# Optimization experiments

Measured on AMD Instinct MI355X. Metric: run time of the kernel, lower is better.

## Reference

```python
import jax, jax.numpy as jnp
import numpy as np

N = 4096      # num nodes
FIN = 256     # num_in_features
H = 8         # num_of_heads
F = 64        # num_out_features per head
NEG = -1e9    # additive mask value for non-edges


def setup_inputs() -> dict:
    key = jax.random.key(0)
    ks = jax.random.split(key, 7)
    x = jax.random.normal(ks[0], (N, FIN), dtype=jnp.float32)
    adj = jax.random.bernoulli(ks[1], 0.01, (N, N)) | jnp.eye(N, dtype=bool)
    connectivity_mask = jnp.where(adj, 0.0, NEG).astype(jnp.float32)
    # Xavier-uniform-ish scaled params
    W = jax.random.normal(ks[2], (H * F, FIN), dtype=jnp.float32) * np.float32(1.0 / np.sqrt(FIN))
    a_src = jax.random.normal(ks[3], (1, H, F), dtype=jnp.float32) * np.float32(0.1)
    a_tgt = jax.random.normal(ks[4], (1, H, F), dtype=jnp.float32) * np.float32(0.1)
    skip_W = jax.random.normal(ks[5], (H * F, FIN), dtype=jnp.float32) * np.float32(1.0 / np.sqrt(FIN))
    bias = jnp.zeros((H * F,), dtype=jnp.float32)
    return {"x": x, "connectivity_mask": connectivity_mask, "W": W,
            "a_src": a_src, "a_tgt": a_tgt, "skip_W": skip_W, "bias": bias}


def reference(x, connectivity_mask, W, a_src, a_tgt, skip_W, bias):
    # linear_proj (no bias), view to [N, H, F]   (dropout omitted: eval mode)
    proj = (x @ W.T).reshape(N, H, F)
    # per-head scalar scores: [N, H] -> [H, N, 1] and [H, 1, N]
    s_src = jnp.sum(proj * a_src, axis=-1).T[:, :, None]   # [H, N, 1]
    s_tgt = jnp.sum(proj * a_tgt, axis=-1).T[:, None, :]   # [H, 1, N]
    scores = jax.nn.leaky_relu(s_src + s_tgt, negative_slope=0.2)  # [H, N, N]
    alpha = jax.nn.softmax(scores + connectivity_mask[None, :, :], axis=-1)
    # weighted aggregation: bmm(alpha, proj^T) then permute back to [N, H, F]
    out = jnp.einsum('hij,jhf->ihf', alpha, proj)
    # skip connection (dims differ: F_in=256 vs H*F output per head) -> skip_proj
    out = out + (x @ skip_W.T).reshape(N, H, F)
    # concat heads, add bias, ELU activation
    out = out.reshape(N, H * F) + bias
    return jax.nn.elu(out)
```

## Files before the change

### kernel.cpp

```cpp
#include <hip/hip_runtime.h>
#include <hip/hip_bf16.h>

#define NN 4096
#define FIN 256
#define NH 8
#define NF 64
#define HF 512
#define MAXD 128

typedef __attribute__((ext_vector_type(4))) float f32x4;
typedef unsigned short u16;
typedef unsigned int u32;

__device__ __forceinline__ u16 f2bf(float x) {
    u32 u = __float_as_uint(x);
    u += 0x7fffu + ((u >> 16) & 1u);
    return (u16)(u >> 16);
}

__global__ __launch_bounds__(256) void gemm64(
    const float* __restrict__ X,
    const float* __restrict__ B0, const float* __restrict__ B1,
    float* __restrict__ C0, float* __restrict__ C1,
    u16* __restrict__ projh)
{
    const float* Bp = blockIdx.z ? B1 : B0;
    float* Cp = blockIdx.z ? C1 : C0;
    const int bm = blockIdx.y * 64, bn = blockIdx.x * 64;
    __shared__ float As[32][68];
    __shared__ float Bs[32][68];
    const int t = threadIdx.x;
    const int tx = t & 15, ty = t >> 4;
    const int r = t >> 2, kq = (t & 3) * 8;
    f32x4 acc[4] = {};
    for (int k0 = 0; k0 < FIN; k0 += 32) {
        const float4 av0 = *(const float4*)&X[(bm + r) * FIN + k0 + kq];
        const float4 av1 = *(const float4*)&X[(bm + r) * FIN + k0 + kq + 4];
        const float4 bv0 = *(const float4*)&Bp[(bn + r) * FIN + k0 + kq];
        const float4 bv1 = *(const float4*)&Bp[(bn + r) * FIN + k0 + kq + 4];
        __syncthreads();
        As[kq+0][r]=av0.x; As[kq+1][r]=av0.y; As[kq+2][r]=av0.z; As[kq+3][r]=av0.w;
        As[kq+4][r]=av1.x; As[kq+5][r]=av1.y; As[kq+6][r]=av1.z; As[kq+7][r]=av1.w;
        Bs[kq+0][r]=bv0.x; Bs[kq+1][r]=bv0.y; Bs[kq+2][r]=bv0.z; Bs[kq+3][r]=bv0.w;
        Bs[kq+4][r]=bv1.x; Bs[kq+5][r]=bv1.y; Bs[kq+6][r]=bv1.z; Bs[kq+7][r]=bv1.w;
        __syncthreads();
        #pragma unroll
        for (int k = 0; k < 32; ++k) {
            const f32x4 a4 = *(const f32x4*)&As[k][ty * 4];
            const f32x4 b4 = *(const f32x4*)&Bs[k][tx * 4];
            acc[0] += a4.x * b4;
            acc[1] += a4.y * b4;
            acc[2] += a4.z * b4;
            acc[3] += a4.w * b4;
        }
    }
    #pragma unroll
    for (int i = 0; i < 4; ++i)
        *(f32x4*)&Cp[(size_t)(bm + ty * 4 + i) * HF + bn + tx * 4] = acc[i];
    if (blockIdx.z == 0) {
        #pragma unroll
        for (int i = 0; i < 4; ++i) {
            union { u16 h[4]; uint2 v; } pk;
            #pragma unroll
            for (int q = 0; q < 4; ++q) pk.h[q] = f2bf(acc[i][q]);
            *(uint2*)&projh[(size_t)(bm + ty * 4 + i) * HF + bn + tx * 4] = pk.v;
        }
    }
}

__global__ __launch_bounds__(256) void s_kernel(
    const float* __restrict__ proj, const float* __restrict__ a_src,
    const float* __restrict__ a_tgt, float* __restrict__ s_src,
    float* __restrict__ s_tgt)
{
    const int wg = (blockIdx.x * 256 + threadIdx.x) >> 6;
    const int lane = threadIdx.x & 63;
    const int i = wg >> 3, h = wg & 7;
    const float v = proj[(size_t)i * HF + h * NF + lane];
    float ps = v * a_src[h * NF + lane];
    float pt = v * a_tgt[h * NF + lane];
    #pragma unroll
    for (int off = 32; off; off >>= 1) {
        ps += __shfl_xor(ps, off);
        pt += __shfl_xor(pt, off);
    }
    if (lane == 0) { s_src[h * NN + i] = ps; s_tgt[h * NN + i] = pt; }
}

__global__ __launch_bounds__(256) void sparse_attn(
    const float* __restrict__ mask, const u16* __restrict__ projh,
    const float* __restrict__ s_src, const float* __restrict__ s_tgt,
    const float* __restrict__ skipv, const float* __restrict__ bias,
    float* __restrict__ out)
{
    const int i = blockIdx.x;
    const int t = threadIdx.x;
    __shared__ int nbr[MAXD];
    __shared__ float alpha_s[NH][MAXD];
    __shared__ int cnt_s;
    if (t == 0) cnt_s = 0;
    __syncthreads();

    const float4* mrow = (const float4*)&mask[(size_t)i * NN];
    #pragma unroll
    for (int it = 0; it < 4; ++it) {
        const float4 v = mrow[it * 256 + t];
        const int j0 = (it * 256 + t) * 4;
        if (v.x > -0.5f) { int p = atomicAdd(&cnt_s, 1); if (p < MAXD) nbr[p] = j0; }
        if (v.y > -0.5f) { int p = atomicAdd(&cnt_s, 1); if (p < MAXD) nbr[p] = j0 + 1; }
        if (v.z > -0.5f) { int p = atomicAdd(&cnt_s, 1); if (p < MAXD) nbr[p] = j0 + 2; }
        if (v.w > -0.5f) { int p = atomicAdd(&cnt_s, 1); if (p < MAXD) nbr[p] = j0 + 3; }
    }
    __syncthreads();
    const int cnt = min(cnt_s, MAXD);

    {
        const int h = t >> 5, l = t & 31;
        const float ss = s_src[h * NN + i];
        float sc[4]; float m = -1e30f;
        #pragma unroll
        for (int q = 0; q < 4; ++q) {
            const int k = l + 32 * q;
            if (k < cnt) {
                float s = ss + s_tgt[h * NN + nbr[k]];
                s = s > 0.f ? s : 0.2f * s;
                sc[q] = s; m = fmaxf(m, s);
            } else sc[q] = -1e30f;
        }
        #pragma unroll
        for (int off = 16; off; off >>= 1) m = fmaxf(m, __shfl_xor(m, off));
        float p[4]; float psum = 0.f;
        #pragma unroll
        for (int q = 0; q < 4; ++q) {
            p[q] = exp2f((sc[q] - m) * 1.4426950408889634f);
            psum += p[q];
        }
        #pragma unroll
        for (int off = 16; off; off >>= 1) psum += __shfl_xor(psum, off);
        const float inv = 1.0f / psum;
        #pragma unroll
        for (int q = 0; q < 4; ++q) {
            const int k = l + 32 * q;
            if (k < cnt) alpha_s[h][k] = p[q] * inv;
        }
    }
    __syncthreads();

    const int w = t >> 6, lane = t & 63;
    const int c = w * 128 + lane * 2;
    const int head = c >> 6;
    const u32* ph = (const u32*)projh;
    const int cidx = c >> 1;
    float acc0 = 0.f, acc1 = 0.f;
    int k = 0;
    for (; k + 2 <= cnt; k += 2) {
        const int j0 = nbr[k], j1 = nbr[k + 1];
        const float a0 = alpha_s[head][k], a1 = alpha_s[head][k + 1];
        const u32 v0 = ph[(size_t)j0 * 256 + cidx];
        const u32 v1 = ph[(size_t)j1 * 256 + cidx];
        acc0 += a0 * __uint_as_float(v0 << 16);
        acc1 += a0 * __uint_as_float(v0 & 0xffff0000u);
        acc0 += a1 * __uint_as_float(v1 << 16);
        acc1 += a1 * __uint_as_float(v1 & 0xffff0000u);
    }
    if (k < cnt) {
        const int j0 = nbr[k];
        const float a0 = alpha_s[head][k];
        const u32 v0 = ph[(size_t)j0 * 256 + cidx];
        acc0 += a0 * __uint_as_float(v0 << 16);
        acc1 += a0 * __uint_as_float(v0 & 0xffff0000u);
    }

    const float2 sk = *(const float2*)&skipv[(size_t)i * HF + c];
    const float2 bs = *(const float2*)&bias[c];
    float o0 = acc0 + sk.x + bs.x;
    float o1 = acc1 + sk.y + bs.y;
    o0 = o0 > 0.f ? o0 : expm1f(o0);
    o1 = o1 > 0.f ? o1 : expm1f(o1);
    *(float2*)&out[(size_t)i * HF + c] = make_float2(o0, o1);
}

extern "C" void kernel_launch(void* const* d_in, const int* in_sizes, int n_in,
                              void* d_out, int out_size, void* d_ws, size_t ws_size,
                              hipStream_t stream)
{
    (void)in_sizes; (void)n_in; (void)out_size; (void)ws_size;
    const float* x     = (const float*)d_in[0];
    const float* mask  = (const float*)d_in[1];
    const float* W     = (const float*)d_in[2];
    const float* a_src = (const float*)d_in[3];
    const float* a_tgt = (const float*)d_in[4];
    const float* skW   = (const float*)d_in[5];
    const float* bias  = (const float*)d_in[6];
    float* out = (float*)d_out;

    char* ws = (char*)d_ws;
    float* proj  = (float*)(ws);
    float* skipv = (float*)(ws + (8u << 20));
    u16*   projh = (u16*)(ws + (16u << 20));
    float* s_src = (float*)(ws + (20u << 20));
    float* s_tgt = (float*)(ws + (20u << 20) + 262144);

    gemm64<<<dim3(8, 64, 2), 256, 0, stream>>>(x, W, skW, proj, skipv, projh);
    s_kernel<<<dim3(8192), 256, 0, stream>>>(proj, a_src, a_tgt, s_src, s_tgt);
    sparse_attn<<<dim3(4096), 256, 0, stream>>>(mask, projh, s_src, s_tgt,
                                                skipv, bias, out);
}
```

Measured before the change: 169.3 us.

## Use bf16 MFMA GEMM, split mask scan from aggregation, unroll gather loop

Converts x and both weight matrices to bf16 and replaces the fp32 SIMT GEMM with a double-buffered MFMA 16x16x32 bf16 GEMM that loads tiles with global_load_lds. The fp32 proj buffer is dropped and the score kernel reads the bf16 projection instead. The mask scan moves into its own kernel that writes neighbour lists, and the aggregation loop is unrolled by 8 with padded entries so more gathers are in flight. This adds a conversion pass and bf16 rounding of the GEMM inputs, which lowers precision of proj, skip and the scores.

```diff
diff --git a/kernel.cpp b/kernel.cpp
--- a/kernel.cpp
+++ b/kernel.cpp
@@ -9,74 +9,140 @@
 #define MAXD 128
 
 typedef __attribute__((ext_vector_type(4))) float f32x4;
+typedef __attribute__((ext_vector_type(8))) short short8;
 typedef unsigned short u16;
 typedef unsigned int u32;
+
+union Frag { uint4 u; short8 s; };
 
 __device__ __forceinline__ u16 f2bf(float x) {
     u32 u = __float_as_uint(x);
     u += 0x7fffu + ((u >> 16) & 1u);
     return (u16)(u >> 16);
 }
-
-__global__ __launch_bounds__(256) void gemm64(
-    const float* __restrict__ X,
-    const float* __restrict__ B0, const float* __restrict__ B1,
-    float* __restrict__ C0, float* __restrict__ C1,
-    u16* __restrict__ projh)
-{
-    const float* Bp = blockIdx.z ? B1 : B0;
-    float* Cp = blockIdx.z ? C1 : C0;
-    const int bm = blockIdx.y * 64, bn = blockIdx.x * 64;
-    __shared__ float As[32][68];
-    __shared__ float Bs[32][68];
+__device__ __forceinline__ float bf2f(u32 lo16) {
+    return __uint_as_float(lo16 << 16);
+}
+
+__global__ __launch_bounds__(256) void cvt_kernel(
+    const float* __restrict__ x, const float* __restrict__ W,
+    const float* __restrict__ skW,
+    u16* __restrict__ xh, u16* __restrict__ Wh, u16* __restrict__ skWh)
+{
+    const int gid = blockIdx.x * 256 + threadIdx.x;
+    const float* src; u16* dst; int off;
+    if (gid < 131072)      { src = x;   dst = xh;   off = gid; }
+    else if (gid < 147456) { src = W;   dst = Wh;   off = gid - 131072; }
+    else                   { src = skW; dst = skWh; off = gid - 147456; }
+    const int e = off * 8;
+    const float4 a = *(const float4*)&src[e];
+    const float4 b = *(const float4*)&src[e + 4];
+    union { u16 h[8]; uint4 v; } pk;
+    pk.h[0]=f2bf(a.x); pk.h[1]=f2bf(a.y); pk.h[2]=f2bf(a.z); pk.h[3]=f2bf(a.w);
+    pk.h[4]=f2bf(b.x); pk.h[5]=f2bf(b.y); pk.h[6]=f2bf(b.z); pk.h[7]=f2bf(b.w);
+    *(uint4*)&dst[e] = pk.v;
+}
+
+__global__ __launch_bounds__(256) void gemm_mfma(
+    const u16* __restrict__ xh, const u16* __restrict__ Wh,
+    const u16* __restrict__ skWh,
+    u16* __restrict__ projh, float* __restrict__ skipv)
+{
+    const int z = blockIdx.z;
+    const u16* Bg = z ? skWh : Wh;
+    const int bm = blockIdx.y * 128, bn = blockIdx.x * 128;
+    __shared__ u16 lds[2][2][8192];
     const int t = threadIdx.x;
-    const int tx = t & 15, ty = t >> 4;
-    const int r = t >> 2, kq = (t & 3) * 8;
-    f32x4 acc[4] = {};
-    for (int k0 = 0; k0 < FIN; k0 += 32) {
-        const float4 av0 = *(const float4*)&X[(bm + r) * FIN + k0 + kq];
-        const float4 av1 = *(const float4*)&X[(bm + r) * FIN + k0 + kq + 4];
-        const float4 bv0 = *(const float4*)&Bp[(bn + r) * FIN + k0 + kq];
-        const float4 bv1 = *(const float4*)&Bp[(bn + r) * FIN + k0 + kq + 4];
+    const int w = t >> 6, lane = t & 63;
+    const int wm = w >> 1, wn = w & 1;
+    const int l15 = lane & 15, lk = lane >> 4;
+
+    f32x4 acc[4][4] = {};
+
+    auto stage = [&](int buf, int ks) {
+        const int k0 = ks * 64;
+        #pragma unroll
+        for (int q = 0; q < 4; ++q) {
+            const int s = q * 256 + t;
+            const int kk = s >> 9, fr = (s >> 6) & 7;
+            const int row = bm + fr * 16 + l15;
+            const int kel = k0 + kk * 32 + lk * 8;
+            u16* ldst = &lds[buf][0][(q * 256 + w * 64) * 8];
+            __builtin_amdgcn_global_load_lds(
+                (const __attribute__((address_space(1))) u32*)&xh[row * FIN + kel],
+                (__attribute__((address_space(3))) u32*)ldst, 16, 0, 0);
+        }
+        #pragma unroll
+        for (int q = 0; q < 4; ++q) {
+            const int s = q * 256 + t;
+            const int kk = s >> 9, fr = (s >> 6) & 7;
+            const int row = bn + fr * 16 + l15;
+            const int kel = k0 + kk * 32 + lk * 8;
+            u16* ldst = &lds[buf][1][(q * 256 + w * 64) * 8];
+            __builtin_amdgcn_global_load_lds(
+                (const __attribute__((address_space(1))) u32*)&Bg[row * FIN + kel],
+                (__attribute__((address_space(3))) u32*)ldst, 16, 0, 0);
+        }
+    };
+    auto compute = [&](int buf) {
+        const uint4* Ab = (const uint4*)&lds[buf][0][0];
+        const uint4* Bb = (const uint4*)&lds[buf][1][0];
+        #pragma unroll
+        for (int kk = 0; kk < 2; ++kk) {
+            Frag a[4], b[4];
+            #pragma unroll
+            for (int m = 0; m < 4; ++m) a[m].u = Ab[(kk * 8 + wm * 4 + m) * 64 + lane];
+            #pragma unroll
+            for (int n = 0; n < 4; ++n) b[n].u = Bb[(kk * 8 + wn * 4 + n) * 64 + lane];
+            #pragma unroll
+            for (int m = 0; m < 4; ++m)
+                #pragma unroll
+                for (int n = 0; n < 4; ++n)
+                    acc[m][n] = __builtin_amdgcn_mfma_f32_16x16x32_bf16(
+                        a[m].s, b[n].s, acc[m][n], 0, 0, 0);
+        }
+    };
+
+    stage(0, 0);
+    asm volatile("s_waitcnt vmcnt(0)" ::: "memory");
+    __syncthreads();
+    int buf = 0;
+    for (int ks = 0; ks < 4; ++ks) {
+        if (ks < 3) stage(buf ^ 1, ks + 1);
+        compute(buf);
+        asm volatile("s_waitcnt vmcnt(0)" ::: "memory");
         __syncthreads();
-        As[kq+0][r]=av0.x; As[kq+1][r]=av0.y; As[kq+2][r]=av0.z; As[kq+3][r]=av0.w;
-        As[kq+4][r]=av1.x; As[kq+5][r]=av1.y; As[kq+6][r]=av1.z; As[kq+7][r]=av1.w;
-        Bs[kq+0][r]=bv0.x; Bs[kq+1][r]=bv0.y; Bs[kq+2][r]=bv0.z; Bs[kq+3][r]=bv0.w;
-        Bs[kq+4][r]=bv1.x; Bs[kq+5][r]=bv1.y; Bs[kq+6][r]=bv1.z; Bs[kq+7][r]=bv1.w;
-        __syncthreads();
-        #pragma unroll
-        for (int k = 0; k < 32; ++k) {
-            const f32x4 a4 = *(const f32x4*)&As[k][ty * 4];
-            const f32x4 b4 = *(const f32x4*)&Bs[k][tx * 4];
-            acc[0] += a4.x * b4;
-            acc[1] += a4.y * b4;
-            acc[2] += a4.z * b4;
-            acc[3] += a4.w * b4;
-        }
-    }
+        buf ^= 1;
+    }
+
     #pragma unroll
-    for (int i = 0; i < 4; ++i)
-        *(f32x4*)&Cp[(size_t)(bm + ty * 4 + i) * HF + bn + tx * 4] = acc[i];
-    if (blockIdx.z == 0) {
-        #pragma unroll
-        for (int i = 0; i < 4; ++i) {
-            union { u16 h[4]; uint2 v; } pk;
-            #pragma unroll
-            for (int q = 0; q < 4; ++q) pk.h[q] = f2bf(acc[i][q]);
-            *(uint2*)&projh[(size_t)(bm + ty * 4 + i) * HF + bn + tx * 4] = pk.v;
+    for (int m = 0; m < 4; ++m) {
+        const int r0 = bm + wm * 64 + m * 16 + lk * 4;
+        #pragma unroll
+        for (int n = 0; n < 4; ++n) {
+            const int c = bn + wn * 64 + n * 16 + l15;
+            if (z == 0) {
+                #pragma unroll
+                for (int rr = 0; rr < 4; ++rr)
+                    projh[(size_t)(r0 + rr) * HF + c] = f2bf(acc[m][n][rr]);
+            } else {
+                #pragma unroll
+                for (int rr = 0; rr < 4; ++rr)
+                    skipv[(size_t)(r0 + rr) * HF + c] = acc[m][n][rr];
+            }
         }
     }
 }
 
 __global__ __launch_bounds__(256) void s_kernel(
-    const float* __restrict__ proj, const float* __restrict__ a_src,
+    const u16* __restrict__ projh, const float* __restrict__ a_src,
     const float* __restrict__ a_tgt, float* __restrict__ s_src,
     float* __restrict__ s_tgt)
 {
     const int wg = (blockIdx.x * 256 + threadIdx.x) >> 6;
     const int lane = threadIdx.x & 63;
     const int i = wg >> 3, h = wg & 7;
-    const float v = proj[(size_t)i * HF + h * NF + lane];
+    const float v = bf2f(projh[(size_t)i * HF + h * NF + lane]);
     float ps = v * a_src[h * NF + lane];
     float pt = v * a_tgt[h * NF + lane];
     #pragma unroll
@@ -87,32 +153,48 @@
     if (lane == 0) { s_src[h * NN + i] = ps; s_tgt[h * NN + i] = pt; }
 }
 
-__global__ __launch_bounds__(256) void sparse_attn(
-    const float* __restrict__ mask, const u16* __restrict__ projh,
-    const float* __restrict__ s_src, const float* __restrict__ s_tgt,
-    const float* __restrict__ skipv, const float* __restrict__ bias,
-    float* __restrict__ out)
-{
-    const int i = blockIdx.x;
-    const int t = threadIdx.x;
-    __shared__ int nbr[MAXD];
-    __shared__ float alpha_s[NH][MAXD];
+__global__ __launch_bounds__(256) void scan_kernel(
+    const float* __restrict__ mask, int* __restrict__ cnt_g,
+    int* __restrict__ nbr_g)
+{
+    const int i = blockIdx.x, t = threadIdx.x;
+    __shared__ int nbr_s[MAXD];
     __shared__ int cnt_s;
     if (t == 0) cnt_s = 0;
     __syncthreads();
-
     const float4* mrow = (const float4*)&mask[(size_t)i * NN];
     #pragma unroll
     for (int it = 0; it < 4; ++it) {
         const float4 v = mrow[it * 256 + t];
         const int j0 = (it * 256 + t) * 4;
-        if (v.x > -0.5f) { int p = atomicAdd(&cnt_s, 1); if (p < MAXD) nbr[p] = j0; }
-        if (v.y > -0.5f) { int p = atomicAdd(&cnt_s, 1); if (p < MAXD) nbr[p] = j0 + 1; }
-        if (v.z > -0.5f) { int p = atomicAdd(&cnt_s, 1); if (p < MAXD) nbr[p] = j0 + 2; }
-        if (v.w > -0.5f) { int p = atomicAdd(&cnt_s, 1); if (p < MAXD) nbr[p] = j0 + 3; }
+        if (v.x > -0.5f) { int p = atomicAdd(&cnt_s, 1); if (p < MAXD) nbr_s[p] = j0; }
+        if (v.y > -0.5f) { int p = atomicAdd(&cnt_s, 1); if (p < MAXD) nbr_s[p] = j0 + 1; }
+        if (v.z > -0.5f) { int p = atomicAdd(&cnt_s, 1); if (p < MAXD) nbr_s[p] = j0 + 2; }
+        if (v.w > -0.5f) { int p = atomicAdd(&cnt_s, 1); if (p < MAXD) nbr_s[p] = j0 + 3; }
     }
     __syncthreads();
     const int cnt = min(cnt_s, MAXD);
+    if (t == 0) cnt_g[i] = cnt;
+    if (t < cnt) nbr_g[i * MAXD + t] = nbr_s[t];
+}
+
+__global__ __launch_bounds__(256) void agg_kernel(
+    const u16* __restrict__ projh, const int* __restrict__ cnt_g,
+    const int* __restrict__ nbr_g,
+    const float* __restrict__ s_src, const float* __restrict__ s_tgt,
+    const float* __restrict__ skipv, const float* __restrict__ bias,
+    float* __restrict__ out)
+{
+    const int i = blockIdx.x, t = threadIdx.x;
+    __shared__ int nbr_s[MAXD + 8];
+    __shared__ float alpha_s[NH][MAXD + 8];
+    __shared__ int cnt_sh;
+    if (t == 0) cnt_sh = cnt_g[i];
+    __syncthreads();
+    const int cnt = cnt_sh;
+    if (t < cnt) nbr_s[t] = nbr_g[i * MAXD + t];
+    if (t < 8) nbr_s[cnt + t] = i;
+    __syncthreads();
 
     {
         const int h = t >> 5, l = t & 31;
@@ -122,7 +204,7 @@
         for (int q = 0; q < 4; ++q) {
             const int k = l + 32 * q;
             if (k < cnt) {
-                float s = ss + s_tgt[h * NN + nbr[k]];
+                float s = ss + s_tgt[h * NN + nbr_s[k]];
                 s = s > 0.f ? s : 0.2f * s;
                 sc[q] = s; m = fmaxf(m, s);
             } else sc[q] = -1e30f;
@@ -143,32 +225,28 @@
             const int k = l + 32 * q;
             if (k < cnt) alpha_s[h][k] = p[q] * inv;
         }
+        if (l < 8) alpha_s[h][cnt + l] = 0.f;
     }
     __syncthreads();
 
     const int w = t >> 6, lane = t & 63;
     const int c = w * 128 + lane * 2;
-    const int head = c >> 6;
+    const int head = c >> 6, cidx = c >> 1;
     const u32* ph = (const u32*)projh;
-    const int cidx = c >> 1;
     float acc0 = 0.f, acc1 = 0.f;
-    int k = 0;
-    for (; k + 2 <= cnt; k += 2) {
-        const int j0 = nbr[k], j1 = nbr[k + 1];
-        const float a0 = alpha_s[head][k], a1 = alpha_s[head][k + 1];
-        const u32 v0 = ph[(size_t)j0 * 256 + cidx];
-        const u32 v1 = ph[(size_t)j1 * 256 + cidx];
-        acc0 += a0 * __uint_as_float(v0 << 16);
-        acc1 += a0 * __uint_as_float(v0 & 0xffff0000u);
-        acc0 += a1 * __uint_as_float(v1 << 16);
-        acc1 += a1 * __uint_as_float(v1 & 0xffff0000u);
-    }
-    if (k < cnt) {
-        const int j0 = nbr[k];
-        const float a0 = alpha_s[head][k];
-        const u32 v0 = ph[(size_t)j0 * 256 + cidx];
-        acc0 += a0 * __uint_as_float(v0 << 16);
-        acc1 += a0 * __uint_as_float(v0 & 0xffff0000u);
+    const int kmax = (cnt + 7) & ~7;
+    for (int k0 = 0; k0 < kmax; k0 += 8) {
+        u32 v[8]; float av[8];
+        #pragma unroll
+        for (int u = 0; u < 8; ++u) {
+            v[u] = ph[(size_t)nbr_s[k0 + u] * 256 + cidx];
+            av[u] = alpha_s[head][k0 + u];
+        }
+        #pragma unroll
+        for (int u = 0; u < 8; ++u) {
+            acc0 += av[u] * bf2f(v[u] & 0xffffu);
+            acc1 += av[u] * __uint_as_float(v[u] & 0xffff0000u);
+        }
     }
 
     const float2 sk = *(const float2*)&skipv[(size_t)i * HF + c];
@@ -195,14 +273,20 @@
     float* out = (float*)d_out;
 
     char* ws = (char*)d_ws;
-    float* proj  = (float*)(ws);
-    float* skipv = (float*)(ws + (8u << 20));
-    u16*   projh = (u16*)(ws + (16u << 20));
-    float* s_src = (float*)(ws + (20u << 20));
-    float* s_tgt = (float*)(ws + (20u << 20) + 262144);
-
-    gemm64<<<dim3(8, 64, 2), 256, 0, stream>>>(x, W, skW, proj, skipv, projh);
-    s_kernel<<<dim3(8192), 256, 0, stream>>>(proj, a_src, a_tgt, s_src, s_tgt);
-    sparse_attn<<<dim3(4096), 256, 0, stream>>>(mask, projh, s_src, s_tgt,
-                                                skipv, bias, out);
-}
+    u16*   xh    = (u16*)(ws);
+    u16*   Wh    = (u16*)(ws + 0x200000);
+    u16*   skWh  = (u16*)(ws + 0x240000);
+    u16*   projh = (u16*)(ws + 0x400000);
+    float* skipv = (float*)(ws + 0x800000);
+    float* s_src = (float*)(ws + 0x1000000);
+    float* s_tgt = (float*)(ws + 0x1020000);
+    int*   cnt_g = (int*)(ws + 0x1040000);
+    int*   nbr_g = (int*)(ws + 0x1048000);
+
+    scan_kernel<<<dim3(4096), 256, 0, stream>>>(mask, cnt_g, nbr_g);
+    cvt_kernel<<<dim3(640), 256, 0, stream>>>(x, W, skW, xh, Wh, skWh);
+    gemm_mfma<<<dim3(4, 32, 2), 256, 0, stream>>>(xh, Wh, skWh, projh, skipv);
+    s_kernel<<<dim3(8192), 256, 0, stream>>>(projh, a_src, a_tgt, s_src, s_tgt);
+    agg_kernel<<<dim3(4096), 256, 0, stream>>>(projh, cnt_g, nbr_g,
+                                               s_src, s_tgt, skipv, bias, out);
+}
```

New measurement: 145.4 us. 14.1% less time.
